# Kernel optimization log

Hardware: AMD Instinct MI355X
Metric: run time of the kernel (lower is better)

Reference implementation:

```python
import jax, jax.numpy as jnp
import numpy as np

B, T, K = 512, 512, 128


def setup_inputs() -> dict:
    key = jax.random.key(0)
    k1, k2, k3, k4, k5 = jax.random.split(key, 5)
    emissions = jax.random.normal(k1, (B, T, K), dtype=jnp.float32)
    tags = jax.random.randint(k2, (B, T), 0, K, dtype=jnp.int64)
    mask = jnp.ones((B, T), dtype=jnp.bool_)
    # learned CRF params, init uniform(-0.1, 0.1) as in reset_parameters
    transitions = jax.random.uniform(k3, (K, K), jnp.float32, -0.1, 0.1)
    start_transitions = jax.random.uniform(k4, (K,), jnp.float32, -0.1, 0.1)
    end_transitions = jax.random.uniform(k5, (K,), jnp.float32, -0.1, 0.1)
    return {
        "emissions": emissions,
        "tags": tags,
        "mask": mask,
        "transitions": transitions,
        "start_transitions": start_transitions,
        "end_transitions": end_transitions,
    }


def _log_partition(emissions, mask, transitions, start_transitions, end_transitions):
    # emissions: [T, B, K] time-major; mask: [T, B]
    log_alpha0 = start_transitions[None, :] + emissions[0]  # [B, K]

    def step(log_alpha, inp):
        em_t, m_t = inp  # [B, K], [B]
        # inner[b, i, j] = log_alpha[b, i] + transitions[i, j] + em_t[b, j]
        inner = log_alpha[:, :, None] + transitions[None, :, :] + em_t[:, None, :]
        new = jax.nn.logsumexp(inner, axis=1)  # [B, K]
        log_alpha = jnp.where(m_t[:, None], new, log_alpha)
        return log_alpha, None

    log_alpha, _ = jax.lax.scan(step, log_alpha0, (emissions[1:], mask[1:]))
    log_alpha = log_alpha + end_transitions[None, :]
    return jax.nn.logsumexp(log_alpha, axis=1)  # [B]


def _gold_score(emissions, tags, mask, transitions, start_transitions, end_transitions):
    # time-major emissions [T, B, K], tags/mask [T, B]
    maskf = mask.astype(emissions.dtype)
    score = start_transitions[tags[0]]  # [B]
    # emission scores: gather tag emission at each step, masked
    em = jnp.take_along_axis(emissions, tags[:, :, None], axis=2)[:, :, 0]  # [T, B]
    score = score + jnp.sum(em * maskf, axis=0)
    # transition scores: transitions[tags[i], tags[i-1]] (note [to, from] order, as in source)
    trans = transitions[tags[1:], tags[:-1]]  # [T-1, B]
    score = score + jnp.sum(trans * maskf[1:], axis=0)
    last_idx = jnp.sum(mask.astype(jnp.int32), axis=0) - 1  # [B]
    last_tags = jnp.take_along_axis(tags, last_idx[None, :], axis=0)[0]  # [B]
    score = score + end_transitions[last_tags]
    return score


def reference(emissions, tags, mask, transitions, start_transitions, end_transitions):
    # batch_first=True -> transpose to time-major
    em = jnp.transpose(emissions, (1, 0, 2))  # [T, B, K]
    tg = jnp.transpose(tags, (1, 0))  # [T, B]
    mk = jnp.transpose(mask, (1, 0))  # [T, B]
    log_num = _gold_score(em, tg, mk, transitions, start_transitions, end_transitions)
    log_den = _log_partition(em, mk, transitions, start_transitions, end_transitions)
    return -jnp.mean(log_num - log_den)
```

## Files before the change

### kernel.cpp

```cpp
#include <hip/hip_runtime.h>

#define K 128
#define T 512
#define BB 512
#define PADB 20

typedef float f32x2 __attribute__((ext_vector_type(2)));
typedef float f32x4 __attribute__((ext_vector_type(4)));

#define LDS_BARRIER() asm volatile("s_waitcnt lgkmcnt(0)\ns_barrier" ::: "memory")

template <int CTRL>
__device__ __forceinline__ float qperm(float x) {
    return __int_as_float(__builtin_amdgcn_update_dpp(
        0, __float_as_int(x), CTRL, 0xF, 0xF, true));
}
#define QXOR1   0xB1
#define QXOR2   0x4E
#define HMIRROR 0x141

__global__ __launch_bounds__(512, 4) void mega_kernel(
    const float* __restrict__ em, const int* __restrict__ tags,
    const float* __restrict__ trans, const float* __restrict__ startt,
    const float* __restrict__ endt,
    float* __restrict__ log_den, float* __restrict__ log_num)
{
    const int bid  = blockIdx.x;
    const int kind = (bid ^ (bid >> 8)) & 1;
    const int b    = bid >> 1;
    const int tid  = threadIdx.x;

    __shared__ __align__(16) float ebuf[2][8 * PADB];
    __shared__ float sred[K];
    __shared__ float gs[8];

    if (kind) {
        const int* tg = tags + (size_t)b * T;
        const float* emb = em + (size_t)b * T * K;
        int   tag = tg[tid];
        float s   = emb[(size_t)tid * K + tag];
        if (tid >= 1) s += trans[tag * K + tg[tid - 1]];
#pragma unroll
        for (int off = 32; off >= 1; off >>= 1) s += __shfl_xor(s, off);
        if ((tid & 63) == 0) gs[tid >> 6] = s;
        __syncthreads();
        if (tid == 0) {
            float tot = ((gs[0] + gs[1]) + (gs[2] + gs[3]))
                      + ((gs[4] + gs[5]) + (gs[6] + gs[7]));
            log_num[b] = tot + startt[tg[0]] + endt[tg[T - 1]];
        }
        return;
    }

    const int iblk = tid & 7;
    const int jg   = tid >> 3;
    const int j    = 2 * jg + (iblk & 1);
    const bool writer = (iblk < 2);

    f32x2 Ec[16];
    {
        const volatile float* Tv = trans;
        const int r0 = iblk * 16, c0 = 2 * jg;
#pragma unroll
        for (int m = 0; m < 8; ++m) {
            float t0 = Tv[(size_t)(r0 + 2 * m)     * K + c0];
            float t1 = Tv[(size_t)(r0 + 2 * m + 1) * K + c0];
            float t2 = Tv[(size_t)(r0 + 2 * m)     * K + c0 + 1];
            float t3 = Tv[(size_t)(r0 + 2 * m + 1) * K + c0 + 1];
            Ec[m].x     = __expf(t0);  Ec[m].y     = __expf(t1);
            Ec[8 + m].x = __expf(t2);  Ec[8 + m].y = __expf(t3);
        }
    }

    const float* emb = em + (size_t)b * T * K;
    const float* emj = emb + j;

    if (tid < K)
        ebuf[0][(tid >> 4) * PADB + (tid & 15)] = __expf(startt[tid] + emb[tid]);

    float ex = 0.f, r1 = 0.f, r2 = 0.f, r3 = 0.f;
    if (writer) {
        ex = __expf(emj[(size_t)1 * K]);
        r1 = emj[(size_t)2 * K];
        r2 = emj[(size_t)3 * K];
        r3 = emj[(size_t)4 * K];
    }

    LDS_BARRIER();

    int   ksum = 0;
    float ycur = 0.f;

    for (int t = 1; t < T; ++t) {
        const float* RB = ebuf[(t - 1) & 1];
        float*       WB = ebuf[t & 1];

        float u0 = RB[0];
        const float* rb = RB + iblk * PADB;

        f32x2 a0 = {0.f, 0.f}, a1 = {0.f, 0.f};
#pragma unroll
        for (int r = 0; r < 4; ++r) {
            f32x4 ev = *reinterpret_cast<const f32x4*>(rb + (r << 2));
            f32x2 plo; plo.x = ev.x; plo.y = ev.y;
            f32x2 phi; phi.x = ev.z; phi.y = ev.w;
            a0 += plo * Ec[2 * r];      a0 += phi * Ec[2 * r + 1];
            a1 += plo * Ec[8 + 2 * r];  a1 += phi * Ec[8 + 2 * r + 1];
        }
        float y0 = a0.x + a0.y;
        float y1 = a1.x + a1.y;

        y0 += qperm<QXOR1>(y0);   y1 += qperm<QXOR1>(y1);
        y0 += qperm<QXOR2>(y0);   y1 += qperm<QXOR2>(y1);
        y0 += qperm<HMIRROR>(y0); y1 += qperm<HMIRROR>(y1);

        int   k  = (int)((__float_as_uint(u0) >> 23) & 255u) - 126;
        float sc = __uint_as_float((unsigned)(127 - k) << 23);
        ksum += k;

        if (writer) {
            float yown = (iblk & 1) ? y1 : y0;
            ycur = yown * (ex * sc);
            WB[(j >> 4) * PADB + (j & 15)] = ycur;
            ex = __expf(r1);
            r1 = r2; r2 = r3;
            int tn = t + 4; if (tn > T - 1) tn = T - 1;
            r3 = emj[(size_t)tn * K];
        }

        LDS_BARRIER();
    }

    if (writer) sred[j] = ycur * __expf(endt[j]);
    __syncthreads();
    if (tid < 64) {
        float v = sred[tid] + sred[tid + 64];
#pragma unroll
        for (int off = 32; off >= 1; off >>= 1) v += __shfl_xor(v, off);
        if (tid == 0)
            log_den[b] = (float)((double)ksum * 0.6931471805599453) + __logf(v);
    }
}

__global__ __launch_bounds__(512) void reduce_kernel(
    const float* __restrict__ log_num, const float* __restrict__ log_den,
    float* __restrict__ out)
{
    __shared__ float buf[BB];
    const int i = threadIdx.x;
    buf[i] = log_num[i] - log_den[i];
    __syncthreads();
#pragma unroll
    for (int sft = 256; sft >= 1; sft >>= 1) {
        if (i < sft) buf[i] += buf[i + sft];
        __syncthreads();
    }
    if (i == 0) out[0] = -buf[0] / (float)BB;
}

extern "C" void kernel_launch(void* const* d_in, const int* in_sizes, int n_in,
                              void* d_out, int out_size, void* d_ws, size_t ws_size,
                              hipStream_t stream)
{
    const float* em     = (const float*)d_in[0];
    const int*   tags   = (const int*)d_in[1];
    const float* trans  = (const float*)d_in[3];
    const float* startt = (const float*)d_in[4];
    const float* endt   = (const float*)d_in[5];

    float* ws      = (float*)d_ws;
    float* log_den = ws;
    float* log_num = ws + BB;
    float* out     = (float*)d_out;

    mega_kernel<<<2 * BB, 512, 0, stream>>>(em, tags, trans, startt, endt,
                                            log_den, log_num);
    reduce_kernel<<<1, BB, 0, stream>>>(log_num, log_den, out);
}
```

Before: 240.0 us.

## Process two batch sequences per block with packed f32x2 forward recursion

Each forward-algorithm block now advances two batch elements at once, packing their alpha vectors as f32x2 in LDS and duplicating the exp(transitions) coefficients so packed FMAs serve both sequences. The partition is reworked to 16 row-groups of 8 with 4 output columns per thread, which adds one more DPP reduction level. Halving the number of recurrence blocks halves the total count of serial per-step barriers and LDS round trips, spreading their cost over two sequences. The cost is more registers per thread (launch bounds lowered to 2 blocks), fewer blocks in flight, and a longer chain of work per step.

New measurement: 317.0 us. 1.32x slower.

```diff
diff --git a/kernel.cpp b/kernel.cpp
--- a/kernel.cpp
+++ b/kernel.cpp
@@ -3,7 +3,7 @@
 #define K 128
 #define T 512
 #define BB 512
-#define PADB 20
+#define SP 10
 
 typedef float f32x2 __attribute__((ext_vector_type(2)));
 typedef float f32x4 __attribute__((ext_vector_type(4)));
@@ -18,23 +18,23 @@
 #define QXOR1   0xB1
 #define QXOR2   0x4E
 #define HMIRROR 0x141
-
-__global__ __launch_bounds__(512, 4) void mega_kernel(
+#define RMIRROR 0x140
+
+__global__ __launch_bounds__(512, 2) void mega_kernel(
     const float* __restrict__ em, const int* __restrict__ tags,
     const float* __restrict__ trans, const float* __restrict__ startt,
     const float* __restrict__ endt,
     float* __restrict__ log_den, float* __restrict__ log_num)
 {
-    const int bid  = blockIdx.x;
-    const int kind = (bid ^ (bid >> 8)) & 1;
-    const int b    = bid >> 1;
-    const int tid  = threadIdx.x;
-
-    __shared__ __align__(16) float ebuf[2][8 * PADB];
-    __shared__ float sred[K];
+    const int bid = blockIdx.x;
+    const int tid = threadIdx.x;
+
+    __shared__ __align__(16) f32x2 st2[2][16 * SP];
+    __shared__ f32x2 sredP[K];
     __shared__ float gs[8];
 
-    if (kind) {
+    if (bid >= BB / 2) {
+        const int b = bid - BB / 2;
         const int* tg = tags + (size_t)b * T;
         const float* emb = em + (size_t)b * T * K;
         int   tag = tg[tid];
@@ -52,93 +52,134 @@
         return;
     }
 
-    const int iblk = tid & 7;
-    const int jg   = tid >> 3;
-    const int j    = 2 * jg + (iblk & 1);
-    const bool writer = (iblk < 2);
-
-    f32x2 Ec[16];
+    const int ib = tid & 15;
+    const int jg = tid >> 4;
+    const int j  = 4 * jg + (ib & 3);
+    const bool writer = (ib < 4);
+
+    f32x2 Epk[32];
     {
         const volatile float* Tv = trans;
-        const int r0 = iblk * 16, c0 = 2 * jg;
-#pragma unroll
-        for (int m = 0; m < 8; ++m) {
-            float t0 = Tv[(size_t)(r0 + 2 * m)     * K + c0];
-            float t1 = Tv[(size_t)(r0 + 2 * m + 1) * K + c0];
-            float t2 = Tv[(size_t)(r0 + 2 * m)     * K + c0 + 1];
-            float t3 = Tv[(size_t)(r0 + 2 * m + 1) * K + c0 + 1];
-            Ec[m].x     = __expf(t0);  Ec[m].y     = __expf(t1);
-            Ec[8 + m].x = __expf(t2);  Ec[8 + m].y = __expf(t3);
-        }
-    }
-
-    const float* emb = em + (size_t)b * T * K;
-    const float* emj = emb + j;
-
-    if (tid < K)
-        ebuf[0][(tid >> 4) * PADB + (tid & 15)] = __expf(startt[tid] + emb[tid]);
-
-    float ex = 0.f, r1 = 0.f, r2 = 0.f, r3 = 0.f;
+        const int r0 = ib * 8, c0 = jg * 4;
+#pragma unroll
+        for (int c = 0; c < 4; ++c)
+#pragma unroll
+            for (int r = 0; r < 8; ++r) {
+                float e = __expf(Tv[(size_t)(r0 + r) * K + c0 + c]);
+                Epk[c * 8 + r].x = e;
+                Epk[c * 8 + r].y = e;
+            }
+    }
+
+    const float* embA = em + (size_t)(2 * bid)     * T * K;
+    const float* embB = em + (size_t)(2 * bid + 1) * T * K;
+    const float* emjA = embA + j;
+    const float* emjB = embB + j;
+
+    if (tid < K) {
+        f32x2 v;
+        v.x = __expf(startt[tid] + embA[tid]);
+        v.y = __expf(startt[tid] + embB[tid]);
+        st2[0][(tid >> 3) * SP + (tid & 7)] = v;
+    }
+
+    float exA = 0.f, rA1 = 0.f, rA2 = 0.f, rA3 = 0.f;
+    float exB = 0.f, rB1 = 0.f, rB2 = 0.f, rB3 = 0.f;
     if (writer) {
-        ex = __expf(emj[(size_t)1 * K]);
-        r1 = emj[(size_t)2 * K];
-        r2 = emj[(size_t)3 * K];
-        r3 = emj[(size_t)4 * K];
+        exA = __expf(emjA[(size_t)1 * K]);
+        rA1 = emjA[(size_t)2 * K]; rA2 = emjA[(size_t)3 * K]; rA3 = emjA[(size_t)4 * K];
+        exB = __expf(emjB[(size_t)1 * K]);
+        rB1 = emjB[(size_t)2 * K]; rB2 = emjB[(size_t)3 * K]; rB3 = emjB[(size_t)4 * K];
     }
 
     LDS_BARRIER();
 
-    int   ksum = 0;
-    float ycur = 0.f;
+    int   ksumA = 0, ksumB = 0;
+    f32x2 ycur = {0.f, 0.f};
 
     for (int t = 1; t < T; ++t) {
-        const float* RB = ebuf[(t - 1) & 1];
-        float*       WB = ebuf[t & 1];
-
-        float u0 = RB[0];
-        const float* rb = RB + iblk * PADB;
-
-        f32x2 a0 = {0.f, 0.f}, a1 = {0.f, 0.f};
-#pragma unroll
-        for (int r = 0; r < 4; ++r) {
-            f32x4 ev = *reinterpret_cast<const f32x4*>(rb + (r << 2));
-            f32x2 plo; plo.x = ev.x; plo.y = ev.y;
-            f32x2 phi; phi.x = ev.z; phi.y = ev.w;
-            a0 += plo * Ec[2 * r];      a0 += phi * Ec[2 * r + 1];
-            a1 += plo * Ec[8 + 2 * r];  a1 += phi * Ec[8 + 2 * r + 1];
-        }
-        float y0 = a0.x + a0.y;
-        float y1 = a1.x + a1.y;
-
-        y0 += qperm<QXOR1>(y0);   y1 += qperm<QXOR1>(y1);
-        y0 += qperm<QXOR2>(y0);   y1 += qperm<QXOR2>(y1);
-        y0 += qperm<HMIRROR>(y0); y1 += qperm<HMIRROR>(y1);
-
-        int   k  = (int)((__float_as_uint(u0) >> 23) & 255u) - 126;
-        float sc = __uint_as_float((unsigned)(127 - k) << 23);
-        ksum += k;
+        const f32x2* RB = st2[(t - 1) & 1];
+        f32x2*       WB = st2[t & 1];
+
+        f32x2 u0 = RB[0];
+        const f32x2* rb = RB + ib * SP;
+
+        f32x4 q0 = *reinterpret_cast<const f32x4*>(rb + 0);
+        f32x4 q1 = *reinterpret_cast<const f32x4*>(rb + 2);
+        f32x4 q2 = *reinterpret_cast<const f32x4*>(rb + 4);
+        f32x4 q3 = *reinterpret_cast<const f32x4*>(rb + 6);
+        f32x2 e0; e0.x = q0.x; e0.y = q0.y;
+        f32x2 e1; e1.x = q0.z; e1.y = q0.w;
+        f32x2 e2; e2.x = q1.x; e2.y = q1.y;
+        f32x2 e3; e3.x = q1.z; e3.y = q1.w;
+        f32x2 e4; e4.x = q2.x; e4.y = q2.y;
+        f32x2 e5; e5.x = q2.z; e5.y = q2.w;
+        f32x2 e6; e6.x = q3.x; e6.y = q3.y;
+        f32x2 e7; e7.x = q3.z; e7.y = q3.w;
+
+        f32x2 a0 = e0 * Epk[ 0]; a0 += e1 * Epk[ 1]; a0 += e2 * Epk[ 2]; a0 += e3 * Epk[ 3];
+        a0 += e4 * Epk[ 4]; a0 += e5 * Epk[ 5]; a0 += e6 * Epk[ 6]; a0 += e7 * Epk[ 7];
+        f32x2 a1 = e0 * Epk[ 8]; a1 += e1 * Epk[ 9]; a1 += e2 * Epk[10]; a1 += e3 * Epk[11];
+        a1 += e4 * Epk[12]; a1 += e5 * Epk[13]; a1 += e6 * Epk[14]; a1 += e7 * Epk[15];
+        f32x2 a2 = e0 * Epk[16]; a2 += e1 * Epk[17]; a2 += e2 * Epk[18]; a2 += e3 * Epk[19];
+        a2 += e4 * Epk[20]; a2 += e5 * Epk[21]; a2 += e6 * Epk[22]; a2 += e7 * Epk[23];
+        f32x2 a3 = e0 * Epk[24]; a3 += e1 * Epk[25]; a3 += e2 * Epk[26]; a3 += e3 * Epk[27];
+        a3 += e4 * Epk[28]; a3 += e5 * Epk[29]; a3 += e6 * Epk[30]; a3 += e7 * Epk[31];
+
+        f32x2 tv;
+#define RED(LVL)                                                     \
+        tv.x = qperm<LVL>(a0.x); tv.y = qperm<LVL>(a0.y); a0 += tv;   \
+        tv.x = qperm<LVL>(a1.x); tv.y = qperm<LVL>(a1.y); a1 += tv;   \
+        tv.x = qperm<LVL>(a2.x); tv.y = qperm<LVL>(a2.y); a2 += tv;   \
+        tv.x = qperm<LVL>(a3.x); tv.y = qperm<LVL>(a3.y); a3 += tv;
+        RED(QXOR1)
+        RED(QXOR2)
+        RED(HMIRROR)
+        RED(RMIRROR)
+#undef RED
+
+        int kA = (int)((__float_as_uint(u0.x) >> 23) & 255u) - 126;
+        int kB = (int)((__float_as_uint(u0.y) >> 23) & 255u) - 126;
+        f32x2 sc;
+        sc.x = __uint_as_float((unsigned)(127 - kA) << 23);
+        sc.y = __uint_as_float((unsigned)(127 - kB) << 23);
+        ksumA += kA; ksumB += kB;
+
+        f32x2 s1 = (ib & 1) ? a1 : a0;
+        f32x2 s2 = (ib & 1) ? a3 : a2;
+        f32x2 yown = (ib & 2) ? s2 : s1;
+        f32x2 expk; expk.x = exA; expk.y = exB;
+        ycur = yown * (expk * sc);
 
         if (writer) {
-            float yown = (iblk & 1) ? y1 : y0;
-            ycur = yown * (ex * sc);
-            WB[(j >> 4) * PADB + (j & 15)] = ycur;
-            ex = __expf(r1);
-            r1 = r2; r2 = r3;
+            WB[(j >> 3) * SP + (j & 7)] = ycur;
+            exA = __expf(rA1); rA1 = rA2; rA2 = rA3;
+            exB = __expf(rB1); rB1 = rB2; rB2 = rB3;
             int tn = t + 4; if (tn > T - 1) tn = T - 1;
-            r3 = emj[(size_t)tn * K];
+            rA3 = emjA[(size_t)tn * K];
+            rB3 = emjB[(size_t)tn * K];
         }
 
         LDS_BARRIER();
     }
 
-    if (writer) sred[j] = ycur * __expf(endt[j]);
+    if (writer) {
+        float ee = __expf(endt[j]);
+        f32x2 eep; eep.x = ee; eep.y = ee;
+        sredP[j] = ycur * eep;
+    }
     __syncthreads();
     if (tid < 64) {
-        float v = sred[tid] + sred[tid + 64];
-#pragma unroll
-        for (int off = 32; off >= 1; off >>= 1) v += __shfl_xor(v, off);
-        if (tid == 0)
-            log_den[b] = (float)((double)ksum * 0.6931471805599453) + __logf(v);
+        f32x2 v = sredP[tid] + sredP[tid + 64];
+#pragma unroll
+        for (int off = 32; off >= 1; off >>= 1) {
+            v.x += __shfl_xor(v.x, off);
+            v.y += __shfl_xor(v.y, off);
+        }
+        if (tid == 0) {
+            log_den[2 * bid]     = (float)((double)ksumA * 0.6931471805599453) + __logf(v.x);
+            log_den[2 * bid + 1] = (float)((double)ksumB * 0.6931471805599453) + __logf(v.y);
+        }
     }
 }
 
@@ -173,7 +214,7 @@
     float* log_num = ws + BB;
     float* out     = (float*)d_out;
 
-    mega_kernel<<<2 * BB, 512, 0, stream>>>(em, tags, trans, startt, endt,
-                                            log_den, log_num);
+    mega_kernel<<<BB / 2 + BB, 512, 0, stream>>>(em, tags, trans, startt, endt,
+                                                 log_den, log_num);
     reduce_kernel<<<1, BB, 0, stream>>>(log_num, log_den, out);
 }
```

## Split CRF forward recursion into concurrent forward and backward halves meeting midway

Applied to the files above, without the earlier changes.

The 511-step sequential forward recursion is split in two. One 256-thread half of the block runs the forward alpha recursion from t=0, and the other half runs a backward beta recursion (using transposed transitions) from t=T-1. Both meet in the middle, so the serial chain is roughly half as long. The partition is then the dot product of alpha and beta at the meeting point, with the log-scale exponents from both halves added together. Each thread now does four output columns with twice the register-held transition exponentials, which raises register pressure and per-step work per thread.

Measured after the change: 217.9 us (median of 3 runs). 9.2% less time.

```diff
diff --git a/kernel.cpp b/kernel.cpp
--- a/kernel.cpp
+++ b/kernel.cpp
@@ -30,9 +30,10 @@
     const int b    = bid >> 1;
     const int tid  = threadIdx.x;
 
-    __shared__ __align__(16) float ebuf[2][8 * PADB];
-    __shared__ float sred[K];
+    __shared__ __align__(16) float stF[2][8 * PADB];
+    __shared__ __align__(16) float stB[2][8 * PADB];
     __shared__ float gs[8];
+    __shared__ int   iks[2];
 
     if (kind) {
         const int* tg = tags + (size_t)b * T;
@@ -52,38 +53,56 @@
         return;
     }
 
-    const int iblk = tid & 7;
-    const int jg   = tid >> 3;
-    const int j    = 2 * jg + (iblk & 1);
-    const bool writer = (iblk < 2);
-
-    f32x2 Ec[16];
+    const int half = tid >> 8;
+    const int h    = tid & 255;
+    const int ib   = h & 7;
+    const int jg   = h >> 3;
+    const int own  = 4 * jg + (ib & 3);
+    const bool writer = (ib < 4);
+    const int wpos = (own >> 4) * PADB + (own & 15);
+
+    f32x2 Ec[32];
     {
         const volatile float* Tv = trans;
-        const int r0 = iblk * 16, c0 = 2 * jg;
-#pragma unroll
-        for (int m = 0; m < 8; ++m) {
-            float t0 = Tv[(size_t)(r0 + 2 * m)     * K + c0];
-            float t1 = Tv[(size_t)(r0 + 2 * m + 1) * K + c0];
-            float t2 = Tv[(size_t)(r0 + 2 * m)     * K + c0 + 1];
-            float t3 = Tv[(size_t)(r0 + 2 * m + 1) * K + c0 + 1];
-            Ec[m].x     = __expf(t0);  Ec[m].y     = __expf(t1);
-            Ec[8 + m].x = __expf(t2);  Ec[8 + m].y = __expf(t3);
-        }
+        const int r0 = ib * 16, c0 = jg * 4;
+#pragma unroll
+        for (int c = 0; c < 4; ++c)
+#pragma unroll
+            for (int p = 0; p < 8; ++p) {
+                float x0, x1;
+                if (half == 0) {
+                    x0 = Tv[(size_t)(r0 + 2 * p)     * K + c0 + c];
+                    x1 = Tv[(size_t)(r0 + 2 * p + 1) * K + c0 + c];
+                } else {
+                    x0 = Tv[(size_t)(c0 + c) * K + r0 + 2 * p];
+                    x1 = Tv[(size_t)(c0 + c) * K + r0 + 2 * p + 1];
+                }
+                Ec[c * 8 + p].x = __expf(x0);
+                Ec[c * 8 + p].y = __expf(x1);
+            }
     }
 
     const float* emb = em + (size_t)b * T * K;
-    const float* emj = emb + j;
-
-    if (tid < K)
-        ebuf[0][(tid >> 4) * PADB + (tid & 15)] = __expf(startt[tid] + emb[tid]);
+    const float* emo = emb + own;
+
+    if (tid < K) {
+        const int x = tid;
+        stF[0][(x >> 4) * PADB + (x & 15)] = __expf(startt[x] + emb[x]);
+    } else if (tid >= 256 && tid < 256 + K) {
+        const int x = tid - 256;
+        stB[0][(x >> 4) * PADB + (x & 15)] =
+            __expf(endt[x] + emb[(size_t)(T - 1) * K + x]);
+    }
 
     float ex = 0.f, r1 = 0.f, r2 = 0.f, r3 = 0.f;
     if (writer) {
-        ex = __expf(emj[(size_t)1 * K]);
-        r1 = emj[(size_t)2 * K];
-        r2 = emj[(size_t)3 * K];
-        r3 = emj[(size_t)4 * K];
+        if (half == 0) {
+            ex = __expf(emo[(size_t)1 * K]);
+            r1 = emo[(size_t)2 * K]; r2 = emo[(size_t)3 * K]; r3 = emo[(size_t)4 * K];
+        } else {
+            ex = __expf(emo[(size_t)510 * K]);
+            r1 = emo[(size_t)509 * K]; r2 = emo[(size_t)508 * K]; r3 = emo[(size_t)507 * K];
+        }
     }
 
     LDS_BARRIER();
@@ -91,54 +110,89 @@
     int   ksum = 0;
     float ycur = 0.f;
 
-    for (int t = 1; t < T; ++t) {
-        const float* RB = ebuf[(t - 1) & 1];
-        float*       WB = ebuf[t & 1];
-
-        float u0 = RB[0];
-        const float* rb = RB + iblk * PADB;
-
-        f32x2 a0 = {0.f, 0.f}, a1 = {0.f, 0.f};
-#pragma unroll
-        for (int r = 0; r < 4; ++r) {
-            f32x4 ev = *reinterpret_cast<const f32x4*>(rb + (r << 2));
-            f32x2 plo; plo.x = ev.x; plo.y = ev.y;
-            f32x2 phi; phi.x = ev.z; phi.y = ev.w;
-            a0 += plo * Ec[2 * r];      a0 += phi * Ec[2 * r + 1];
-            a1 += plo * Ec[8 + 2 * r];  a1 += phi * Ec[8 + 2 * r + 1];
+    for (int it = 0; it < 256; ++it) {
+        const bool active = (half == 0) || (it >= 1);
+        const float* RB = (half == 0) ? stF[it & 1]       : stB[(it - 1) & 1];
+        float*       WB = (half == 0) ? stF[(it + 1) & 1] : stB[it & 1];
+
+        if (active) {
+            float u0 = RB[0];
+            const float* rb = RB + ib * PADB;
+
+            f32x4 q0 = *reinterpret_cast<const f32x4*>(rb + 0);
+            f32x4 q1 = *reinterpret_cast<const f32x4*>(rb + 4);
+            f32x4 q2 = *reinterpret_cast<const f32x4*>(rb + 8);
+            f32x4 q3 = *reinterpret_cast<const f32x4*>(rb + 12);
+            f32x2 e0; e0.x = q0.x; e0.y = q0.y;
+            f32x2 e1; e1.x = q0.z; e1.y = q0.w;
+            f32x2 e2; e2.x = q1.x; e2.y = q1.y;
+            f32x2 e3; e3.x = q1.z; e3.y = q1.w;
+            f32x2 e4; e4.x = q2.x; e4.y = q2.y;
+            f32x2 e5; e5.x = q2.z; e5.y = q2.w;
+            f32x2 e6; e6.x = q3.x; e6.y = q3.y;
+            f32x2 e7; e7.x = q3.z; e7.y = q3.w;
+
+            f32x2 a0 = e0 * Ec[ 0]; a0 += e1 * Ec[ 1]; a0 += e2 * Ec[ 2]; a0 += e3 * Ec[ 3];
+            a0 += e4 * Ec[ 4]; a0 += e5 * Ec[ 5]; a0 += e6 * Ec[ 6]; a0 += e7 * Ec[ 7];
+            f32x2 a1 = e0 * Ec[ 8]; a1 += e1 * Ec[ 9]; a1 += e2 * Ec[10]; a1 += e3 * Ec[11];
+            a1 += e4 * Ec[12]; a1 += e5 * Ec[13]; a1 += e6 * Ec[14]; a1 += e7 * Ec[15];
+            f32x2 a2 = e0 * Ec[16]; a2 += e1 * Ec[17]; a2 += e2 * Ec[18]; a2 += e3 * Ec[19];
+            a2 += e4 * Ec[20]; a2 += e5 * Ec[21]; a2 += e6 * Ec[22]; a2 += e7 * Ec[23];
+            f32x2 a3 = e0 * Ec[24]; a3 += e1 * Ec[25]; a3 += e2 * Ec[26]; a3 += e3 * Ec[27];
+            a3 += e4 * Ec[28]; a3 += e5 * Ec[29]; a3 += e6 * Ec[30]; a3 += e7 * Ec[31];
+
+            f32x2 c01, c23;
+            c01.x = a0.x + a0.y;  c01.y = a1.x + a1.y;
+            c23.x = a2.x + a2.y;  c23.y = a3.x + a3.y;
+
+            f32x2 tv;
+            tv.x = qperm<QXOR1>(c01.x);   tv.y = qperm<QXOR1>(c01.y);   c01 += tv;
+            tv.x = qperm<QXOR1>(c23.x);   tv.y = qperm<QXOR1>(c23.y);   c23 += tv;
+            tv.x = qperm<QXOR2>(c01.x);   tv.y = qperm<QXOR2>(c01.y);   c01 += tv;
+            tv.x = qperm<QXOR2>(c23.x);   tv.y = qperm<QXOR2>(c23.y);   c23 += tv;
+            tv.x = qperm<HMIRROR>(c01.x); tv.y = qperm<HMIRROR>(c01.y); c01 += tv;
+            tv.x = qperm<HMIRROR>(c23.x); tv.y = qperm<HMIRROR>(c23.y); c23 += tv;
+
+            int   k  = (int)((__float_as_uint(u0) >> 23) & 255u) - 126;
+            float sc = __uint_as_float((unsigned)(127 - k) << 23);
+            ksum += k;
+
+            float ya   = (ib & 1) ? c01.y : c01.x;
+            float yb   = (ib & 1) ? c23.y : c23.x;
+            float yown = (ib & 2) ? yb : ya;
+            float exu  = (half == 1 && it == 255) ? 1.0f : ex;
+            ycur = yown * (exu * sc);
+
+            if (writer) {
+                WB[wpos] = ycur;
+                ex = __expf(r1);
+                r1 = r2; r2 = r3;
+                if (half == 0) {
+                    int tn = it + 5; if (tn > T - 1) tn = T - 1;
+                    r3 = emo[(size_t)tn * K];
+                } else {
+                    int tn = 507 - it; if (tn < 0) tn = 0;
+                    r3 = emo[(size_t)tn * K];
+                }
+            }
         }
-        float y0 = a0.x + a0.y;
-        float y1 = a1.x + a1.y;
-
-        y0 += qperm<QXOR1>(y0);   y1 += qperm<QXOR1>(y1);
-        y0 += qperm<QXOR2>(y0);   y1 += qperm<QXOR2>(y1);
-        y0 += qperm<HMIRROR>(y0); y1 += qperm<HMIRROR>(y1);
-
-        int   k  = (int)((__float_as_uint(u0) >> 23) & 255u) - 126;
-        float sc = __uint_as_float((unsigned)(127 - k) << 23);
-        ksum += k;
-
-        if (writer) {
-            float yown = (iblk & 1) ? y1 : y0;
-            ycur = yown * (ex * sc);
-            WB[(j >> 4) * PADB + (j & 15)] = ycur;
-            ex = __expf(r1);
-            r1 = r2; r2 = r3;
-            int tn = t + 4; if (tn > T - 1) tn = T - 1;
-            r3 = emj[(size_t)tn * K];
-        }
 
         LDS_BARRIER();
     }
 
-    if (writer) sred[j] = ycur * __expf(endt[j]);
+    if (tid == 0)   iks[0] = ksum;
+    if (tid == 256) iks[1] = ksum;
     __syncthreads();
     if (tid < 64) {
-        float v = sred[tid] + sred[tid + 64];
+        const int x = tid, x2 = tid + 64;
+        const int p1 = (x  >> 4) * PADB + (x  & 15);
+        const int p2 = (x2 >> 4) * PADB + (x2 & 15);
+        float v = stF[0][p1] * stB[1][p1] + stF[0][p2] * stB[1][p2];
 #pragma unroll
         for (int off = 32; off >= 1; off >>= 1) v += __shfl_xor(v, off);
         if (tid == 0)
-            log_den[b] = (float)((double)ksum * 0.6931471805599453) + __logf(v);
+            log_den[b] = (float)((double)(iks[0] + iks[1]) * 0.6931471805599453)
+                       + __logf(v);
     }
 }
 
```
